# Kernel optimization log

Hardware: AMD Instinct MI355X
Metric: run time of the kernel (lower is better)

## Reference

```python
import jax, jax.numpy as jnp
import numpy as np

WS = 16          # window_size
N = WS * WS      # tokens per window
H = 8            # num_heads
HD = 64          # head_dim
DIM = 512
EPEG_K = 15
PAD = EPEG_K // 2


def _relative_position_index(ws):
    coords = np.stack(np.meshgrid(np.arange(ws), np.arange(ws), indexing='ij'))  # (2, ws, ws)
    flat = coords.reshape(2, -1)                                                 # (2, N)
    rel = flat[:, :, None] - flat[:, None, :]                                    # (2, N, N)
    rel = rel.transpose(1, 2, 0).astype(np.int64)                                # (N, N, 2)
    rel[..., 0] += ws - 1
    rel[..., 1] += ws - 1
    rel[..., 0] *= 2 * ws - 1
    return rel.sum(-1)                                                           # (N, N)

REL_IDX = jnp.asarray(_relative_position_index(WS), dtype=jnp.int32)


def setup_inputs() -> dict:
    key = jax.random.key(0)
    ks = jax.random.split(key, 8)
    B_ = 128
    x = jax.random.normal(ks[0], (B_, N, DIM), dtype=jnp.float32)
    qkv_w = jax.random.normal(ks[1], (3 * H * HD, DIM), dtype=jnp.float32) * 0.02
    qkv_b = jnp.zeros((3 * H * HD,), dtype=jnp.float32)
    pe_w = jax.random.normal(ks[2], (H, 1, EPEG_K, 1), dtype=jnp.float32) * 0.02  # depthwise (15,1) conv
    pe_b = jnp.zeros((H,), dtype=jnp.float32)
    rpb_table = jax.random.normal(ks[3], ((2 * WS - 1) * (2 * WS - 1), H), dtype=jnp.float32) * 0.02
    proj_w = jax.random.normal(ks[4], (DIM, H * HD), dtype=jnp.float32) * 0.02
    proj_b = jnp.zeros((DIM,), dtype=jnp.float32)
    return {"x": x, "qkv_w": qkv_w, "qkv_b": qkv_b, "pe_w": pe_w, "pe_b": pe_b,
            "rpb_table": rpb_table, "proj_w": proj_w, "proj_b": proj_b}


def reference(x, qkv_w, qkv_b, pe_w, pe_b, rpb_table, proj_w, proj_b):
    B_, n, _ = x.shape
    scale = HD ** -0.5
    qkv = (x @ qkv_w.T + qkv_b).reshape(B_, n, 3, H, HD).transpose(2, 0, 3, 1, 4)  # (3,B_,H,N,hd)
    q, k, v = qkv[0] * scale, qkv[1], qkv[2]
    attn = jnp.einsum('bhnd,bhmd->bhnm', q, k)                                    # (B_,H,N,N)
    # epeg: depthwise conv (k,1) over the score map, per head
    pe = jax.lax.conv_general_dilated(
        attn, pe_w, window_strides=(1, 1), padding=((PAD, PAD), (0, 0)),
        dimension_numbers=('NCHW', 'OIHW', 'NCHW'), feature_group_count=H)
    attn = attn + pe + pe_b[None, :, None, None]
    bias = rpb_table[REL_IDX.reshape(-1)].reshape(n, n, H).transpose(2, 0, 1)     # (H,N,N)
    attn = jax.nn.softmax(attn + bias[None], axis=-1)
    out = jnp.einsum('bhnm,bhmd->bnhd', attn, v).reshape(B_, n, H * HD)
    return out @ proj_w.T + proj_b
```

## Files before the change

### kernel.cpp

```cpp
#include <hip/hip_runtime.h>


typedef unsigned short u16;
typedef unsigned int u32;
typedef __attribute__((ext_vector_type(8))) short short8;
typedef __attribute__((ext_vector_type(4))) float f32x4;

__device__ __forceinline__ u16 f2bf(float f) {
  union { float f; u32 u; } v; v.f = f;
  return (u16)((v.u + 0x7FFFu + ((v.u >> 16) & 1u)) >> 16);
}
__device__ __forceinline__ float bf2f(u16 s) {
  union { u32 u; float f; } v; v.u = ((u32)s) << 16;
  return v.f;
}
__device__ __forceinline__ u32 cvtpk(float lo, float hi) {
  u32 r;
  asm("v_cvt_pk_bf16_f32 %0, %1, %2" : "=v"(r) : "v"(lo), "v"(hi));
  return r;
}

__device__ __forceinline__ void gl2lds16(const u16* g, u16* l) {
  __builtin_amdgcn_global_load_lds((const __attribute__((address_space(1))) void*)g,
                                   (__attribute__((address_space(3))) void*)l, 16, 0, 0);
}

__device__ __forceinline__ int fragaddr(int frag, int lane) {
  return (frag * 64 + (lane ^ (frag & 7))) * 8;
}

__global__ __launch_bounds__(256) void cvt_all(
    const float* __restrict__ x, const float* __restrict__ w1f,
    const float* __restrict__ w2f, u16* __restrict__ xo,
    u16* __restrict__ w1o, u16* __restrict__ w2o) {
  const int NX = 4194304, NW1 = 196608, NW2 = 65536;
  int i = blockIdx.x * 256 + threadIdx.x;
  const float* src; u16* dst; int j;
  if (i < NX)                  { src = x;   dst = xo;  j = i; }
  else if (i < NX + NW1)       { src = w1f; dst = w1o; j = i - NX; }
  else if (i < NX + NW1 + NW2) { src = w2f; dst = w2o; j = i - NX - NW1; }
  else return;
  float4 f = ((const float4*)src)[j];
  uint2 o;
  o.x = (u32)f2bf(f.x) | ((u32)f2bf(f.y) << 16);
  o.y = (u32)f2bf(f.z) | ((u32)f2bf(f.w) << 16);
  ((uint2*)dst)[j] = o;
}

__device__ __forceinline__ void gemm256_core(
    const u16* __restrict__ A, const u16* __restrict__ B,
    int m0, int n0, u16* lds, f32x4 acc[8][4]) {
  const int NT = 8;
  int tid = threadIdx.x, wave = tid >> 6, lane = tid & 63;
  int wm = wave >> 2, wn = wave & 3;

  int ch0 = tid, ch1 = tid + 512;
  int row0 = ch0 >> 2, row1 = ch1 >> 2;
  int cg0 = (ch0 & 3) ^ (row0 & 3) ^ ((row0 >> 2) & 3);
  int cg1 = (ch1 & 3) ^ (row1 & 3) ^ ((row1 >> 2) & 3);
  const u16* Ag0 = A + (size_t)(m0 + row0) * 512 + cg0 * 8;
  const u16* Ag1 = A + (size_t)(m0 + row1) * 512 + cg1 * 8;
  const u16* Bg0 = B + (size_t)(n0 + row0) * 512 + cg0 * 8;
  const u16* Bg1 = B + (size_t)(n0 + row1) * 512 + cg1 * 8;
  int ldsu0 = wave * 64 * 8;
  int ldsu1 = (512 + wave * 64) * 8;

  int frag_off = (lane & 15) * 32 +
                 (((lane >> 4) ^ (lane & 3) ^ ((lane >> 2) & 3)) << 3);
  int abase = wm * 4096 + frag_off;
  int bbase = 8192 + wn * 2048 + frag_off;

#define STAGE(h)                                                             \
  do {                                                                       \
    if ((h) < NT * 4) {                                                      \
      int T_ = (h) >> 2, kh_ = ((h) >> 1) & 1, isB_ = (h) & 1;               \
      int ko_ = T_ * 64 + kh_ * 32;                                          \
      u16* d_ = lds + (T_ & 1) * 32768 + kh_ * 16384 + isB_ * 8192;          \
      gl2lds16((isB_ ? Bg0 : Ag0) + ko_, d_ + ldsu0);                        \
      gl2lds16((isB_ ? Bg1 : Ag1) + ko_, d_ + ldsu1);                        \
    }                                                                        \
  } while (0)

#define LDA(dst, mf, kh, p)                                                  \
  dst = *(const short8*)(lds + (p) * 32768 + (kh) * 16384 + abase + (mf) * 512)
#define LDB(dst, nf, kh, p)                                                  \
  dst = *(const short8*)(lds + (p) * 32768 + (kh) * 16384 + bbase + (nf) * 512)

#define MM16(M0)                                                                                   \
  __builtin_amdgcn_s_setprio(1);                                                                   \
  acc[(M0)+0][0] = __builtin_amdgcn_mfma_f32_16x16x32_bf16(b0, a0, acc[(M0)+0][0], 0, 0, 0);       \
  acc[(M0)+0][1] = __builtin_amdgcn_mfma_f32_16x16x32_bf16(b1, a0, acc[(M0)+0][1], 0, 0, 0);       \
  acc[(M0)+0][2] = __builtin_amdgcn_mfma_f32_16x16x32_bf16(b2, a0, acc[(M0)+0][2], 0, 0, 0);       \
  acc[(M0)+0][3] = __builtin_amdgcn_mfma_f32_16x16x32_bf16(b3, a0, acc[(M0)+0][3], 0, 0, 0);       \
  acc[(M0)+1][0] = __builtin_amdgcn_mfma_f32_16x16x32_bf16(b0, a1, acc[(M0)+1][0], 0, 0, 0);       \
  acc[(M0)+1][1] = __builtin_amdgcn_mfma_f32_16x16x32_bf16(b1, a1, acc[(M0)+1][1], 0, 0, 0);       \
  acc[(M0)+1][2] = __builtin_amdgcn_mfma_f32_16x16x32_bf16(b2, a1, acc[(M0)+1][2], 0, 0, 0);       \
  acc[(M0)+1][3] = __builtin_amdgcn_mfma_f32_16x16x32_bf16(b3, a1, acc[(M0)+1][3], 0, 0, 0);       \
  acc[(M0)+2][0] = __builtin_amdgcn_mfma_f32_16x16x32_bf16(b0, a2, acc[(M0)+2][0], 0, 0, 0);       \
  acc[(M0)+2][1] = __builtin_amdgcn_mfma_f32_16x16x32_bf16(b1, a2, acc[(M0)+2][1], 0, 0, 0);       \
  acc[(M0)+2][2] = __builtin_amdgcn_mfma_f32_16x16x32_bf16(b2, a2, acc[(M0)+2][2], 0, 0, 0);       \
  acc[(M0)+2][3] = __builtin_amdgcn_mfma_f32_16x16x32_bf16(b3, a2, acc[(M0)+2][3], 0, 0, 0);       \
  acc[(M0)+3][0] = __builtin_amdgcn_mfma_f32_16x16x32_bf16(b0, a3, acc[(M0)+3][0], 0, 0, 0);       \
  acc[(M0)+3][1] = __builtin_amdgcn_mfma_f32_16x16x32_bf16(b1, a3, acc[(M0)+3][1], 0, 0, 0);       \
  acc[(M0)+3][2] = __builtin_amdgcn_mfma_f32_16x16x32_bf16(b2, a3, acc[(M0)+3][2], 0, 0, 0);       \
  acc[(M0)+3][3] = __builtin_amdgcn_mfma_f32_16x16x32_bf16(b3, a3, acc[(M0)+3][3], 0, 0, 0);       \
  __builtin_amdgcn_s_setprio(0)

  STAGE(0); STAGE(1); STAGE(2); STAGE(3); STAGE(4);
  asm volatile("s_waitcnt vmcnt(6)" ::: "memory");
  __builtin_amdgcn_s_barrier();

#pragma unroll 1
  for (int kt = 0; kt < NT; ++kt) {
    int p = kt & 1;
    int hb = kt * 4 + 5;
    short8 a0, a1, a2, a3, b0, b1, b2, b3;
    LDA(a0, 0, 0, p); LDA(a1, 1, 0, p); LDA(a2, 2, 0, p); LDA(a3, 3, 0, p);
    LDB(b0, 0, 0, p); LDB(b1, 1, 0, p); LDB(b2, 2, 0, p); LDB(b3, 3, 0, p);
    STAGE(hb);
    __builtin_amdgcn_s_barrier();
    asm volatile("s_waitcnt lgkmcnt(0)" ::: "memory");
    MM16(0);
    __builtin_amdgcn_s_barrier();
    LDA(a0, 4, 0, p); LDA(a1, 5, 0, p); LDA(a2, 6, 0, p); LDA(a3, 7, 0, p);
    STAGE(hb + 1);
    __builtin_amdgcn_s_barrier();
    asm volatile("s_waitcnt lgkmcnt(0)" ::: "memory");
    MM16(4);
    if (kt == NT - 1) asm volatile("s_waitcnt vmcnt(0)" ::: "memory");
    else              asm volatile("s_waitcnt vmcnt(6)" ::: "memory");
    __builtin_amdgcn_s_barrier();
    LDA(a0, 0, 1, p); LDA(a1, 1, 1, p); LDA(a2, 2, 1, p); LDA(a3, 3, 1, p);
    LDB(b0, 0, 1, p); LDB(b1, 1, 1, p); LDB(b2, 2, 1, p); LDB(b3, 3, 1, p);
    STAGE(hb + 2);
    __builtin_amdgcn_s_barrier();
    asm volatile("s_waitcnt lgkmcnt(0)" ::: "memory");
    MM16(0);
    __builtin_amdgcn_s_barrier();
    LDA(a0, 4, 1, p); LDA(a1, 5, 1, p); LDA(a2, 6, 1, p); LDA(a3, 7, 1, p);
    STAGE(hb + 3);
    __builtin_amdgcn_s_barrier();
    asm volatile("s_waitcnt lgkmcnt(0)" ::: "memory");
    MM16(4);
    if (kt == NT - 2)     asm volatile("s_waitcnt vmcnt(4)" ::: "memory");
    else if (kt < NT - 2) asm volatile("s_waitcnt vmcnt(6)" ::: "memory");
    __builtin_amdgcn_s_barrier();
  }
#undef STAGE
#undef LDA
#undef LDB
#undef MM16
}

__global__ __launch_bounds__(512, 2) void gemm_qkv256(
    const u16* __restrict__ A, const u16* __restrict__ B,
    const float* __restrict__ qkvb, u16* __restrict__ qb,
    u16* __restrict__ kb, u16* __restrict__ vb) {
  __shared__ __align__(16) u16 lds[65536];
  f32x4 acc[8][4];
#pragma unroll
  for (int a = 0; a < 8; ++a)
#pragma unroll
    for (int c = 0; c < 4; ++c) acc[a][c] = (f32x4){0.f, 0.f, 0.f, 0.f};
  int bid = blockIdx.x;
  int wg = (bid & 7) * 96 + (bid >> 3);
  int m0 = (wg / 6) * 256, n0 = (wg % 6) * 256;
  gemm256_core(A, B, m0, n0, lds, acc);

  int tid = threadIdx.x, wave = tid >> 6, lane = tid & 63;
  int wm = wave >> 2, wn = wave & 3;
  int cx = lane & 15, g = lane >> 4;
  int b = m0 >> 8;

  u16* dstn[4]; float scn[4]; float4 bsn[4];
#pragma unroll
  for (int nf = 0; nf < 4; ++nf) {
    int c0 = n0 + wn * 64 + nf * 16 + g * 4;
    int which = c0 >> 9, cc = c0 & 511, h = cc >> 6, d0 = cc & 63;
    float sc = (which == 0) ? 0.125f : 1.f;
    float4 bv = *(const float4*)(qkvb + c0);
    scn[nf] = sc;
    bsn[nf] = make_float4(bv.x * sc, bv.y * sc, bv.z * sc, bv.w * sc);
    dstn[nf] = (which == 0 ? qb : (which == 1 ? kb : vb)) +
               (size_t)(b * 8 + h) * 16384 + d0;
  }
  int ntok = wm * 128 + cx;
#pragma unroll
  for (int mf = 0; mf < 8; ++mf) {
    int off = (ntok + mf * 16) * 64;
#pragma unroll
    for (int nf = 0; nf < 4; ++nf) {
      f32x4 v = acc[mf][nf];
      u32 w0 = cvtpk(v[0] * scn[nf] + bsn[nf].x, v[1] * scn[nf] + bsn[nf].y);
      u32 w1 = cvtpk(v[2] * scn[nf] + bsn[nf].z, v[3] * scn[nf] + bsn[nf].w);
      *(uint2*)(dstn[nf] + off) = make_uint2(w0, w1);
    }
  }
}

__global__ __launch_bounds__(512, 2) void gemm_proj256(
    const u16* __restrict__ A, const u16* __restrict__ B,
    const float* __restrict__ pb, float* __restrict__ out) {
  __shared__ __align__(16) u16 lds[65536];
  f32x4 acc[8][4];
#pragma unroll
  for (int a = 0; a < 8; ++a)
#pragma unroll
    for (int c = 0; c < 4; ++c) acc[a][c] = (f32x4){0.f, 0.f, 0.f, 0.f};
  int bid = blockIdx.x;
  int wg = (bid & 7) * 32 + (bid >> 3);
  int m0 = (wg >> 1) * 256, n0 = (wg & 1) * 256;
  gemm256_core(A, B, m0, n0, lds, acc);

  int tid = threadIdx.x, wave = tid >> 6, lane = tid & 63;
  int wm = wave >> 2, wn = wave & 3;
  int cx = lane & 15, g = lane >> 4;
  int cb = n0 + wn * 64 + g * 4;
  float4 bv[4];
#pragma unroll
  for (int nf = 0; nf < 4; ++nf) bv[nf] = *(const float4*)(pb + cb + nf * 16);
  int r0 = m0 + wm * 128 + cx;
#pragma unroll
  for (int mf = 0; mf < 8; ++mf) {
    size_t rb = (size_t)(r0 + mf * 16) * 512;
#pragma unroll
    for (int nf = 0; nf < 4; ++nf) {
      f32x4 v = acc[mf][nf];
      float4 o = make_float4(v[0] + bv[nf].x, v[1] + bv[nf].y,
                             v[2] + bv[nf].z, v[3] + bv[nf].w);
      *(float4*)(out + rb + cb + nf * 16) = o;
    }
  }
}

__global__ __launch_bounds__(256) void qconv(u16* __restrict__ qb,
                                             const float* __restrict__ pe_w) {
  __shared__ __align__(16) u16 Ql[256 * 72];
  __shared__ float w[15];
  int bh = blockIdx.x, h = bh & 7, tid = threadIdx.x;
  const uint4* src = (const uint4*)(qb + (size_t)bh * 16384);
#pragma unroll
  for (int it = 0; it < 8; ++it) {
    int idx = tid + it * 256;
    int row = idx >> 3, c = (idx & 7) * 8;
    *(uint4*)(Ql + row * 72 + c) = src[idx];
  }
  if (tid < 15) w[tid] = pe_w[h * 15 + tid] + (tid == 7 ? 1.f : 0.f);
  __syncthreads();
  int dg = (tid & 15) * 4, nb4 = tid >> 4;
  uint2* dst = (uint2*)(qb + (size_t)bh * 16384);
#pragma unroll
  for (int i = 0; i < 16; ++i) {
    int n = nb4 + i * 16;
    float a0 = 0.f, a1 = 0.f, a2 = 0.f, a3 = 0.f;
#pragma unroll
    for (int t = 0; t < 15; ++t) {
      int nn = n + t - 7;
      if (nn < 0 || nn > 255) continue;
      uint2 rv = *(const uint2*)(Ql + nn * 72 + dg);
      float wt = w[t];
      a0 += wt * bf2f(rv.x & 0xffff); a1 += wt * bf2f(rv.x >> 16);
      a2 += wt * bf2f(rv.y & 0xffff); a3 += wt * bf2f(rv.y >> 16);
    }
    uint2 pv;
    pv.x = (u32)f2bf(a0) | ((u32)f2bf(a1) << 16);
    pv.y = (u32)f2bf(a2) | ((u32)f2bf(a3) << 16);
    dst[(n * 64 + dg) >> 2] = pv;
  }
}

__global__ __launch_bounds__(512, 2) void attn_win(
    const u16* __restrict__ qb, const u16* __restrict__ kb,
    const u16* __restrict__ vb, const float* __restrict__ pe_b,
    const float* __restrict__ rpb, u16* __restrict__ attnout) {
  __shared__ __align__(16) u16 KfPs[21504];
  __shared__ __align__(16) u16 Vf[16384];
  __shared__ float biasl[961];

  int bh = blockIdx.x, b = bh >> 3, h = bh & 7;
  int tid = threadIdx.x, wave = tid >> 6, lane = tid & 63;
  int cx = lane & 15, g = lane >> 4;

  const uint4* kg = (const uint4*)(kb + (size_t)bh * 16384);
  const uint4* vg = (const uint4*)(vb + (size_t)bh * 16384);
  const u16* qgb = qb + (size_t)bh * 16384;

  short8 qfr0a = *(const short8*)(qgb + (0 * 128 + wave * 16 + cx) * 64 + g * 8);
  short8 qfr0b = *(const short8*)(qgb + (0 * 128 + wave * 16 + cx) * 64 + 32 + g * 8);
  short8 qfr1a = *(const short8*)(qgb + (1 * 128 + wave * 16 + cx) * 64 + g * 8);
  short8 qfr1b = *(const short8*)(qgb + (1 * 128 + wave * 16 + cx) * 64 + 32 + g * 8);

  uint4 kreg[4];
#pragma unroll
  for (int it = 0; it < 4; ++it) kreg[it] = kg[tid + it * 512];

  u16* Vtmp = KfPs;
#pragma unroll
  for (int it = 0; it < 4; ++it) {
    int idx = tid + it * 512;
    uint4 v = vg[idx];
    int row = idx >> 3, c8 = (idx & 7) * 8;
    *(uint2*)(Vtmp + row * 68 + c8)     = make_uint2(v.x, v.y);
    *(uint2*)(Vtmp + row * 68 + c8 + 4) = make_uint2(v.z, v.w);
  }
  {
    float peb = pe_b[h];
    for (int i = tid; i < 961; i += 512) biasl[i] = rpb[i * 8 + h] + peb;
  }
  __syncthreads();

#pragma unroll
  for (int it = 0; it < 4; ++it) {
    int o = tid + it * 512;
    int frag = o >> 6, lanep = o & 63;
    int d = (frag >> 3) * 16 + (lanep & 15);
    int mb = (frag & 7) * 32 + (lanep >> 4) * 8;
    uint4 pk;
    pk.x = (u32)Vtmp[(mb + 0) * 68 + d] | ((u32)Vtmp[(mb + 1) * 68 + d] << 16);
    pk.y = (u32)Vtmp[(mb + 2) * 68 + d] | ((u32)Vtmp[(mb + 3) * 68 + d] << 16);
    pk.z = (u32)Vtmp[(mb + 4) * 68 + d] | ((u32)Vtmp[(mb + 5) * 68 + d] << 16);
    pk.w = (u32)Vtmp[(mb + 6) * 68 + d] | ((u32)Vtmp[(mb + 7) * 68 + d] << 16);
    *(uint4*)(Vf + (frag * 64 + (lanep ^ (frag & 7))) * 8) = pk;
  }
  __syncthreads();

  u16* Kf = KfPs;
#pragma unroll
  for (int it = 0; it < 4; ++it) {
    int idx = tid + it * 512;
    int n = idx >> 3, k8 = idx & 7;
    int frag = (n >> 4) * 2 + (k8 >> 2);
    int lanep = (n & 15) + 16 * (k8 & 3);
    *(uint4*)(Kf + (frag * 64 + (lanep ^ (frag & 7))) * 8) = kreg[it];
  }
  __syncthreads();

  u16* Psw = KfPs + 16384 + wave * 640;

#pragma unroll
  for (int it2 = 0; it2 < 2; ++it2) {
    short8 qf0 = it2 ? qfr1a : qfr0a;
    short8 qf1 = it2 ? qfr1b : qfr0b;
    int qbase = it2 * 128 + wave * 16;

    float m_run = -1e30f, l_run = 0.f;
    f32x4 oacc[4];
#pragma unroll
    for (int dt = 0; dt < 4; ++dt) oacc[dt] = (f32x4){0.f, 0.f, 0.f, 0.f};

#pragma unroll
    for (int c = 0; c < 2; ++c) {
      f32x4 acc[8];
#pragma unroll
      for (int mt = 0; mt < 8; ++mt) acc[mt] = (f32x4){0.f, 0.f, 0.f, 0.f};
      __builtin_amdgcn_s_setprio(1);
#pragma unroll
      for (int mt = 0; mt < 8; ++mt) {
        int fr = (c * 8 + mt) * 2;
        short8 k0 = *(const short8*)(Kf + fragaddr(fr, lane));
        short8 k1 = *(const short8*)(Kf + fragaddr(fr + 1, lane));
        acc[mt] = __builtin_amdgcn_mfma_f32_16x16x32_bf16(k0, qf0, acc[mt], 0, 0, 0);
        acc[mt] = __builtin_amdgcn_mfma_f32_16x16x32_bf16(k1, qf1, acc[mt], 0, 0, 0);
      }
      __builtin_amdgcn_s_setprio(0);

      int nb = (it2 * 8 + wave - c * 8 + 15) * 31 + cx - g * 4 + 15;
#pragma unroll
      for (int mt = 0; mt < 8; ++mt) {
        const float* bp = biasl + (nb - 31 * mt);
        acc[mt][0] += bp[0];  acc[mt][1] += bp[-1];
        acc[mt][2] += bp[-2]; acc[mt][3] += bp[-3];
      }

      float mx = fmaxf(fmaxf(acc[0][0], acc[0][1]), fmaxf(acc[0][2], acc[0][3]));
#pragma unroll
      for (int mt = 1; mt < 8; ++mt)
        mx = fmaxf(mx, fmaxf(fmaxf(acc[mt][0], acc[mt][1]),
                             fmaxf(acc[mt][2], acc[mt][3])));
      mx = fmaxf(mx, __shfl_xor(mx, 16));
      mx = fmaxf(mx, __shfl_xor(mx, 32));
      float mnew = fmaxf(m_run, mx);
      float al = __expf(m_run - mnew);
      float s = 0.f;
#pragma unroll
      for (int mt = 0; mt < 8; ++mt)
#pragma unroll
        for (int i = 0; i < 4; ++i) {
          float e = __expf(acc[mt][i] - mnew);
          acc[mt][i] = e; s += e;
        }
      s += __shfl_xor(s, 16);
      s += __shfl_xor(s, 32);
      l_run = l_run * al + s;
      m_run = mnew;

#pragma unroll
      for (int dt = 0; dt < 4; ++dt)
#pragma unroll
        for (int i = 0; i < 4; ++i) oacc[dt][i] *= al;

#pragma unroll
      for (int kk = 0; kk < 4; ++kk) {
        u32 w0 = cvtpk(acc[2 * kk][0], acc[2 * kk][1]);
        u32 w1 = cvtpk(acc[2 * kk][2], acc[2 * kk][3]);
        u32 w2 = cvtpk(acc[2 * kk + 1][0], acc[2 * kk + 1][1]);
        u32 w3 = cvtpk(acc[2 * kk + 1][2], acc[2 * kk + 1][3]);
        *(uint2*)(Psw + cx * 40 + g * 4)      = make_uint2(w0, w1);
        *(uint2*)(Psw + cx * 40 + 16 + g * 4) = make_uint2(w2, w3);
        short8 pa = *(const short8*)(Psw + cx * 40 + g * 8);
        __builtin_amdgcn_s_setprio(1);
#pragma unroll
        for (int dt = 0; dt < 4; ++dt) {
          short8 vf = *(const short8*)(Vf + fragaddr(dt * 8 + c * 4 + kk, lane));
          oacc[dt] = __builtin_amdgcn_mfma_f32_16x16x32_bf16(vf, pa, oacc[dt], 0, 0, 0);
        }
        __builtin_amdgcn_s_setprio(0);
      }
    }

    float inv = 1.f / l_run;
    u16* ao = attnout + ((size_t)b * 256 + qbase + cx) * 512 + h * 64;
#pragma unroll
    for (int dt = 0; dt < 4; ++dt) {
      u32 w0 = cvtpk(oacc[dt][0] * inv, oacc[dt][1] * inv);
      u32 w1 = cvtpk(oacc[dt][2] * inv, oacc[dt][3] * inv);
      *(uint2*)(ao + dt * 16 + g * 4) = make_uint2(w0, w1);
    }
  }
}

extern "C" void kernel_launch(void* const* d_in, const int* in_sizes, int n_in,
                              void* d_out, int out_size, void* d_ws, size_t ws_size,
                              hipStream_t stream) {
  const float* x      = (const float*)d_in[0];
  const float* qkv_w  = (const float*)d_in[1];
  const float* qkv_b  = (const float*)d_in[2];
  const float* pe_w   = (const float*)d_in[3];
  const float* pe_b   = (const float*)d_in[4];
  const float* rpb    = (const float*)d_in[5];
  const float* proj_w = (const float*)d_in[6];
  const float* proj_b = (const float*)d_in[7];
  float* out = (float*)d_out;
  char* ws = (char*)d_ws;

  size_t off = 0;
  u16* xbf = (u16*)(ws + off); off += (size_t)16777216 * 2;
  u16* w1  = (u16*)(ws + off); off += (size_t)786432 * 2;
  u16* w2  = (u16*)(ws + off); off += (size_t)262144 * 2;
  u16* qb  = (u16*)(ws + off); off += (size_t)16777216 * 2;
  u16* kb  = (u16*)(ws + off); off += (size_t)16777216 * 2;
  u16* vb  = (u16*)(ws + off); off += (size_t)16777216 * 2;

  hipLaunchKernelGGL(cvt_all, dim3(17408), dim3(256), 0, stream,
                     x, qkv_w, proj_w, xbf, w1, w2);
  hipLaunchKernelGGL(gemm_qkv256, dim3(768), dim3(512), 0, stream,
                     xbf, w1, qkv_b, qb, kb, vb);
  hipLaunchKernelGGL(qconv, dim3(1024), dim3(256), 0, stream, qb, pe_w);
  hipLaunchKernelGGL(attn_win, dim3(1024), dim3(512), 0, stream,
                     qb, kb, vb, pe_b, rpb, xbf);
  hipLaunchKernelGGL(gemm_proj256, dim3(256), dim3(512), 0, stream,
                     xbf, w2, proj_b, out);
}
```

Baseline: 315.8 us.

## Fuse Q token-conv into QKV GEMM epilogue via swizzled LDS staging

Removes the separate qconv kernel by staging each 256x256 QKV GEMM output tile in LDS, then applying the 15-tap token-axis conv (plus identity) to the Q columns directly in the epilogue. K and V tiles are also written back through LDS with 16-byte coalesced stores instead of scattered 8-byte stores. This avoids one full read and write of the Q buffer and a kernel launch. It adds a serial conv epilogue and extra barriers to the GEMM blocks that produce Q, and the bias is now added before scaling rather than pre-scaled.

```diff
diff --git a/kernel.cpp b/kernel.cpp
--- a/kernel.cpp
+++ b/kernel.cpp
@@ -154,8 +154,8 @@
 
 __global__ __launch_bounds__(512, 2) void gemm_qkv256(
     const u16* __restrict__ A, const u16* __restrict__ B,
-    const float* __restrict__ qkvb, u16* __restrict__ qb,
-    u16* __restrict__ kb, u16* __restrict__ vb) {
+    const float* __restrict__ qkvb, const float* __restrict__ pe_w,
+    u16* __restrict__ qb, u16* __restrict__ kb, u16* __restrict__ vb) {
   __shared__ __align__(16) u16 lds[65536];
   f32x4 acc[8][4];
 #pragma unroll
@@ -170,30 +170,74 @@
   int tid = threadIdx.x, wave = tid >> 6, lane = tid & 63;
   int wm = wave >> 2, wn = wave & 3;
   int cx = lane & 15, g = lane >> 4;
+
+  __syncthreads();
+  float sc = (n0 < 512) ? 0.125f : 1.f;
+  float4 bvn[4];
+#pragma unroll
+  for (int nf = 0; nf < 4; ++nf)
+    bvn[nf] = *(const float4*)(qkvb + n0 + wn * 64 + nf * 16 + g * 4);
+#pragma unroll
+  for (int mf = 0; mf < 8; ++mf) {
+    int r = wm * 128 + mf * 16 + cx;
+    int swz = ((r >> 2) & 3) << 1;
+#pragma unroll
+    for (int nf = 0; nf < 4; ++nf) {
+      int c0 = wn * 64 + nf * 16 + g * 4;
+      int c16 = (c0 >> 3) ^ swz;
+      f32x4 v = acc[mf][nf];
+      u32 w0 = cvtpk((v[0] + bvn[nf].x) * sc, (v[1] + bvn[nf].y) * sc);
+      u32 w1 = cvtpk((v[2] + bvn[nf].z) * sc, (v[3] + bvn[nf].w) * sc);
+      *(uint2*)(lds + r * 256 + c16 * 8 + (c0 & 7)) = make_uint2(w0, w1);
+    }
+  }
+  __syncthreads();
+
   int b = m0 >> 8;
-
-  u16* dstn[4]; float scn[4]; float4 bsn[4];
-#pragma unroll
-  for (int nf = 0; nf < 4; ++nf) {
-    int c0 = n0 + wn * 64 + nf * 16 + g * 4;
-    int which = c0 >> 9, cc = c0 & 511, h = cc >> 6, d0 = cc & 63;
-    float sc = (which == 0) ? 0.125f : 1.f;
-    float4 bv = *(const float4*)(qkvb + c0);
-    scn[nf] = sc;
-    bsn[nf] = make_float4(bv.x * sc, bv.y * sc, bv.z * sc, bv.w * sc);
-    dstn[nf] = (which == 0 ? qb : (which == 1 ? kb : vb)) +
-               (size_t)(b * 8 + h) * 16384 + d0;
-  }
-  int ntok = wm * 128 + cx;
-#pragma unroll
-  for (int mf = 0; mf < 8; ++mf) {
-    int off = (ntok + mf * 16) * 64;
-#pragma unroll
-    for (int nf = 0; nf < 4; ++nf) {
-      f32x4 v = acc[mf][nf];
-      u32 w0 = cvtpk(v[0] * scn[nf] + bsn[nf].x, v[1] * scn[nf] + bsn[nf].y);
-      u32 w1 = cvtpk(v[2] * scn[nf] + bsn[nf].z, v[3] * scn[nf] + bsn[nf].w);
-      *(uint2*)(dstn[nf] + off) = make_uint2(w0, w1);
+  int nrow = tid >> 3, dc = tid & 7;
+  if (n0 >= 512) {
+#pragma unroll
+    for (int j = 0; j < 16; ++j) {
+      const int hg = j >> 2;
+      int gcol = n0 + hg * 64;
+      int h = (gcol >> 6) & 7;
+      u16* dst = ((gcol >> 9) == 1 ? kb : vb) + (size_t)(b * 8 + h) * 16384;
+      int n = (j & 3) * 64 + nrow;
+      int c16 = (hg * 8 + dc) ^ (((n >> 2) & 3) << 1);
+      uint4 val = *(const uint4*)(lds + n * 256 + c16 * 8);
+      *(uint4*)(dst + n * 64 + dc * 8) = val;
+    }
+  } else {
+#pragma unroll 1
+    for (int hg = 0; hg < 4; ++hg) {
+      int h = ((n0 + hg * 64) >> 6) & 7;
+      float wv[15];
+#pragma unroll
+      for (int t = 0; t < 15; ++t)
+        wv[t] = pe_w[h * 15 + t] + (t == 7 ? 1.f : 0.f);
+      u16* dst = qb + (size_t)(b * 8 + h) * 16384;
+#pragma unroll
+      for (int jj = 0; jj < 4; ++jj) {
+        int n = jj * 64 + nrow;
+        float a0 = 0.f, a1 = 0.f, a2 = 0.f, a3 = 0.f;
+        float a4 = 0.f, a5 = 0.f, a6 = 0.f, a7 = 0.f;
+#pragma unroll
+        for (int t = 0; t < 15; ++t) {
+          int nn = n + t - 7;
+          if (nn < 0 || nn > 255) continue;
+          int c16 = (hg * 8 + dc) ^ (((nn >> 2) & 3) << 1);
+          uint4 v = *(const uint4*)(lds + nn * 256 + c16 * 8);
+          float wt = wv[t];
+          a0 += wt * bf2f(v.x & 0xffff); a1 += wt * bf2f(v.x >> 16);
+          a2 += wt * bf2f(v.y & 0xffff); a3 += wt * bf2f(v.y >> 16);
+          a4 += wt * bf2f(v.z & 0xffff); a5 += wt * bf2f(v.z >> 16);
+          a6 += wt * bf2f(v.w & 0xffff); a7 += wt * bf2f(v.w >> 16);
+        }
+        uint4 o;
+        o.x = cvtpk(a0, a1); o.y = cvtpk(a2, a3);
+        o.z = cvtpk(a4, a5); o.w = cvtpk(a6, a7);
+        *(uint4*)(dst + n * 64 + dc * 8) = o;
+      }
     }
   }
 }
@@ -230,42 +274,6 @@
                              v[2] + bv[nf].z, v[3] + bv[nf].w);
       *(float4*)(out + rb + cb + nf * 16) = o;
     }
-  }
-}
-
-__global__ __launch_bounds__(256) void qconv(u16* __restrict__ qb,
-                                             const float* __restrict__ pe_w) {
-  __shared__ __align__(16) u16 Ql[256 * 72];
-  __shared__ float w[15];
-  int bh = blockIdx.x, h = bh & 7, tid = threadIdx.x;
-  const uint4* src = (const uint4*)(qb + (size_t)bh * 16384);
-#pragma unroll
-  for (int it = 0; it < 8; ++it) {
-    int idx = tid + it * 256;
-    int row = idx >> 3, c = (idx & 7) * 8;
-    *(uint4*)(Ql + row * 72 + c) = src[idx];
-  }
-  if (tid < 15) w[tid] = pe_w[h * 15 + tid] + (tid == 7 ? 1.f : 0.f);
-  __syncthreads();
-  int dg = (tid & 15) * 4, nb4 = tid >> 4;
-  uint2* dst = (uint2*)(qb + (size_t)bh * 16384);
-#pragma unroll
-  for (int i = 0; i < 16; ++i) {
-    int n = nb4 + i * 16;
-    float a0 = 0.f, a1 = 0.f, a2 = 0.f, a3 = 0.f;
-#pragma unroll
-    for (int t = 0; t < 15; ++t) {
-      int nn = n + t - 7;
-      if (nn < 0 || nn > 255) continue;
-      uint2 rv = *(const uint2*)(Ql + nn * 72 + dg);
-      float wt = w[t];
-      a0 += wt * bf2f(rv.x & 0xffff); a1 += wt * bf2f(rv.x >> 16);
-      a2 += wt * bf2f(rv.y & 0xffff); a3 += wt * bf2f(rv.y >> 16);
-    }
-    uint2 pv;
-    pv.x = (u32)f2bf(a0) | ((u32)f2bf(a1) << 16);
-    pv.y = (u32)f2bf(a2) | ((u32)f2bf(a3) << 16);
-    dst[(n * 64 + dg) >> 2] = pv;
   }
 }
 
@@ -454,8 +462,7 @@
   hipLaunchKernelGGL(cvt_all, dim3(17408), dim3(256), 0, stream,
                      x, qkv_w, proj_w, xbf, w1, w2);
   hipLaunchKernelGGL(gemm_qkv256, dim3(768), dim3(512), 0, stream,
-                     xbf, w1, qkv_b, qb, kb, vb);
-  hipLaunchKernelGGL(qconv, dim3(1024), dim3(256), 0, stream, qb, pe_w);
+                     xbf, w1, qkv_b, pe_w, qb, kb, vb);
   hipLaunchKernelGGL(attn_win, dim3(1024), dim3(512), 0, stream,
                      qb, kb, vb, pe_b, rpb, xbf);
   hipLaunchKernelGGL(gemm_proj256, dim3(256), dim3(512), 0, stream,
```

Result: no change. 317.0 us (+0.4%).
